# Performance work log

Measured on AMD Instinct MI355X. Metric: run time of the kernel, lower is better.

## Reference

```python
import jax, jax.numpy as jnp
import numpy as np

N, E, B, IN, H, T = 50000, 800000, 256, 32, 96, 8
BN_EPS = 1e-5


def setup_inputs() -> dict:
    key = jax.random.key(0)
    ks = jax.random.split(key, 40)
    inp = {}
    inp["x"] = jax.random.normal(ks[0], (N, IN), dtype=jnp.float32)
    inp["edge_index"] = jax.random.randint(ks[1], (2, E), 0, N, dtype=jnp.int64)
    inp["batch"] = jnp.sort(jax.random.randint(ks[2], (N,), 0, B, dtype=jnp.int64))
    inp["r_target"] = jax.random.randint(ks[3], (B,), 0, T, dtype=jnp.int64)
    k = 4
    for i, din in zip((1, 2, 3), (IN, H, H)):
        inp[f"w_in{i}"] = jax.random.normal(ks[k], (din, H), dtype=jnp.float32) / np.sqrt(din); k += 1
        inp[f"b_in{i}"] = jnp.zeros((H,), dtype=jnp.float32)
        inp[f"gamma{i}"] = jnp.ones((H,), dtype=jnp.float32)
        inp[f"beta{i}"] = jnp.zeros((H,), dtype=jnp.float32)
        inp[f"rmean{i}"] = jax.random.normal(ks[k], (H,), dtype=jnp.float32) * 0.1; k += 1
        inp[f"rvar{i}"] = jax.random.uniform(ks[k], (H,), minval=0.5, maxval=1.5, dtype=jnp.float32); k += 1
        inp[f"w_out{i}"] = jax.random.normal(ks[k], (H, H), dtype=jnp.float32) / np.sqrt(H); k += 1
        inp[f"b_out{i}"] = jnp.zeros((H,), dtype=jnp.float32)
    inp["head_w"] = jax.random.normal(ks[k], (T, H), dtype=jnp.float32) / np.sqrt(H)
    inp["head_b"] = jnp.zeros((T,), dtype=jnp.float32)
    return inp


def gin_conv(h, edge_index, w_in, b_in, gamma, beta, rmean, rvar, w_out, b_out):
    # PyG GINConv with eps=0: mlp((1+0)*x + sum_{j in N(i)} x_j)
    agg = jax.ops.segment_sum(h[edge_index[0]], edge_index[1], num_segments=N)
    z = (h + agg) @ w_in + b_in                                   # [N, H]
    z = (z - rmean) * (gamma * jax.lax.rsqrt(rvar + BN_EPS)) + beta  # eval-mode BN
    z = jax.nn.relu(z)
    z = jax.nn.relu(z @ w_out + b_out)
    return z


def reference(x, edge_index, batch, r_target,
              w_in1, b_in1, gamma1, beta1, rmean1, rvar1, w_out1, b_out1,
              w_in2, b_in2, gamma2, beta2, rmean2, rvar2, w_out2, b_out2,
              w_in3, b_in3, gamma3, beta3, rmean3, rvar3, w_out3, b_out3,
              head_w, head_b):
    h = gin_conv(x, edge_index, w_in1, b_in1, gamma1, beta1, rmean1, rvar1, w_out1, b_out1)
    h = jax.nn.relu(h)
    h = gin_conv(h, edge_index, w_in2, b_in2, gamma2, beta2, rmean2, rvar2, w_out2, b_out2)
    h = jax.nn.relu(h)
    h = gin_conv(h, edge_index, w_in3, b_in3, gamma3, beta3, rmean3, rvar3, w_out3, b_out3)
    pooled = jax.ops.segment_sum(h, batch, num_segments=B)        # [B, H]
    # dropout p=0.5 in eval mode -> identity
    w = head_w[r_target]                                          # [B, H] per-sample head
    b = head_b[r_target]                                          # [B]
    return jnp.sum(pooled * w, axis=-1) + b                       # [B]
```

## Files before the change

### kernel.cpp

```cpp
#include <hip/hip_runtime.h>

using u16 = unsigned short;
using u32 = unsigned int;
using u64 = unsigned long long;

typedef __attribute__((ext_vector_type(8))) short bf16x8;
typedef __attribute__((ext_vector_type(4))) float f32x4;

constexpr int Nn  = 50000;
constexpr int Ee  = 800000;
constexpr int Bb  = 256;
constexpr int INF = 32;
constexpr int Hh  = 96;
constexpr float BN_EPS = 1e-5f;

constexpr int BINW = 128;
constexpr int NBIN = (Nn + BINW - 1) / BINW;
constexpr int P1B  = 256;
constexpr int EPB  = Ee / P1B;
constexpr int CAP  = 40;
constexpr int P3IT = P1B * CAP / 256;

constexpr int WROW   = 104;
constexpr int WMAT   = 96 * WROW;
constexpr int WB_TOT = 6 * WMAT;

__device__ __forceinline__ float bfL(u32 u) { return __uint_as_float(u << 16); }
__device__ __forceinline__ float bfH(u32 u) { return __uint_as_float(u & 0xFFFF0000u); }
__device__ __forceinline__ u32 f2bfb(float f) {
    u32 b = __float_as_uint(f);
    return (b + 0x7FFFu + ((b >> 16) & 1u)) >> 16;
}
__device__ __forceinline__ float bf2f(u16 u) { return __uint_as_float(((u32)u) << 16); }

__global__ void x2bf_kernel(const float* __restrict__ x, u16* __restrict__ xb) {
    const int total = Nn * INF / 8;
    for (int i = blockIdx.x * 256 + threadIdx.x; i < total; i += gridDim.x * 256) {
        const float4 a = ((const float4*)x)[2 * i];
        const float4 b = ((const float4*)x)[2 * i + 1];
        uint4 R;
        R.x = f2bfb(a.x) | (f2bfb(a.y) << 16);
        R.y = f2bfb(a.z) | (f2bfb(a.w) << 16);
        R.z = f2bfb(b.x) | (f2bfb(b.y) << 16);
        R.w = f2bfb(b.z) | (f2bfb(b.w) << 16);
        ((uint4*)xb)[i] = R;
    }
}

__global__ void w2bf_kernel(const float* __restrict__ w1i, const float* __restrict__ w1o,
                            const float* __restrict__ w2i, const float* __restrict__ w2o,
                            const float* __restrict__ w3i, const float* __restrict__ w3o,
                            u16* __restrict__ wb) {
    const int i = blockIdx.x * 256 + threadIdx.x;
    if (i >= WB_TOT / 2) return;
    const int mat = i / (WMAT / 2);
    const int rem = i % (WMAT / 2);
    const int j   = rem / (WROW / 2);
    const int k   = (rem % (WROW / 2)) * 2;
    const float* src; int din;
    switch (mat) {
        case 0: src = w1i; din = 32; break;
        case 1: src = w1o; din = 96; break;
        case 2: src = w2i; din = 96; break;
        case 3: src = w2o; din = 96; break;
        case 4: src = w3i; din = 96; break;
        default: src = w3o; din = 96; break;
    }
    const u32 lo = (k     < din) ? f2bfb(src[(long)k * 96 + j])       : 0u;
    const u32 hi = (k + 1 < din) ? f2bfb(src[(long)(k + 1) * 96 + j]) : 0u;
    ((u32*)wb)[i] = lo | (hi << 16);
}

__global__ __launch_bounds__(256)
void p1_bin_kernel(const int* __restrict__ src, const int* __restrict__ dst,
                   u32* __restrict__ binbuf, int* __restrict__ counts,
                   int* __restrict__ bintot) {
    __shared__ int cur[NBIN];
    const int b = blockIdx.x, tid = threadIdx.x;
    for (int k = tid; k < NBIN; k += 256) cur[k] = 0;
    __syncthreads();
    const long e0 = (long)b * EPB;
    for (int i = tid; i < EPB; i += 256) {
        const long e = e0 + i;
        const int d = dst[e];
        const int k = d >> 7;
        const int pos = atomicAdd(&cur[k], 1);
        binbuf[((long)b * NBIN + k) * CAP + pos] = ((u32)(d & 127) << 16) | (u32)src[e];
    }
    __syncthreads();
    for (int k = tid; k < NBIN; k += 256) {
        const int c = cur[k];
        counts[k * P1B + b] = c;
        if (c) atomicAdd(&bintot[k], c);
    }
}

__global__ void p2_binscan_kernel(const int* __restrict__ bintot, int* __restrict__ binbase,
                                  int* __restrict__ rowptr) {
    __shared__ int ps[512];
    const int t = threadIdx.x;
    const int v = (t < NBIN) ? bintot[t] : 0;
    ps[t] = v;
    __syncthreads();
    for (int d = 1; d < 512; d <<= 1) {
        int u = (t >= d) ? ps[t - d] : 0;
        __syncthreads();
        if (t >= d) ps[t] += u;
        __syncthreads();
    }
    if (t < NBIN) binbase[t] = ps[t] - v;
    if (t == 0) rowptr[Nn] = Ee;
}

__global__ __launch_bounds__(256)
void p3_binsort_kernel(const u32* __restrict__ binbuf, const int* __restrict__ counts,
                       const int* __restrict__ binbase, int* __restrict__ rowptr,
                       u16* __restrict__ csr) {
    __shared__ int cnt[P1B];
    __shared__ int lhist[BINW];
    __shared__ int lpref[BINW];
    const int k = blockIdx.x, tid = threadIdx.x;

    for (int b = tid; b < P1B; b += 256) cnt[b] = counts[k * P1B + b];
    if (tid < BINW) lhist[tid] = 0;
    __syncthreads();

    u32 pv[P3IT];
    u64 vmask = 0;
    #pragma unroll
    for (int it = 0; it < P3IT; ++it) {
        const int flat = tid + it * 256;
        const int b = flat / CAP, i = flat % CAP;
        if (i < cnt[b]) {
            const u32 v = binbuf[((long)b * NBIN + k) * CAP + i];
            pv[it] = v;
            vmask |= 1ull << it;
            atomicAdd(&lhist[v >> 16], 1);
        }
    }
    __syncthreads();

    if (tid < BINW) lpref[tid] = lhist[tid];
    __syncthreads();
    for (int d = 1; d < BINW; d <<= 1) {
        int u = 0;
        if (tid < BINW && tid >= d) u = lpref[tid - d];
        __syncthreads();
        if (tid < BINW && tid >= d) lpref[tid] += u;
        __syncthreads();
    }
    if (tid < BINW) lpref[tid] -= lhist[tid];

    const int base = binbase[k];
    const int node = k * BINW + tid;
    if (tid < BINW && node < Nn) rowptr[node] = base + lpref[tid];
    if (tid < BINW) lhist[tid] = 0;
    __syncthreads();

    #pragma unroll
    for (int it = 0; it < P3IT; ++it) {
        if (vmask & (1ull << it)) {
            const u32 v = pv[it];
            const int dl = v >> 16;
            const int pos = base + lpref[dl] + atomicAdd(&lhist[dl], 1);
            csr[pos] = (u16)(v & 0xFFFFu);
        }
    }
}

template<int DIN>
__global__ __launch_bounds__(384, 4)
void layer_kernel(const u16* __restrict__ hsrc, const int* __restrict__ rowptr,
                  const u16* __restrict__ csr,
                  const u16* __restrict__ wbg1, const u16* __restrict__ wbg2,
                  const float* __restrict__ b_in,
                  const float* __restrict__ gamma, const float* __restrict__ beta,
                  const float* __restrict__ rmean, const float* __restrict__ rvar,
                  const float* __restrict__ b_out,
                  u16* __restrict__ out) {
    constexpr int TILE = 32;
    constexpr int XST  = 104;
    __shared__ __align__(16) u16 wT[96 * XST];
    __shared__ __align__(16) u16 xs[TILE * XST];

    const int tid = threadIdx.x;
    const int nbase = blockIdx.x * TILE;

    for (int i = tid; i < 96 * XST / 8; i += 384)
        ((uint4*)wT)[i] = ((const uint4*)wbg1)[i];

    {
        const int grp = tid / 12, ln = tid % 12;
        const int node = nbase + grp;
        if (node < Nn) {
            const int e0 = rowptr[node], e1 = rowptr[node + 1];
            if constexpr (DIN == 96) {
                const uint4* h4 = (const uint4*)hsrc;
                float a0, a1, a2, a3, a4, a5, a6, a7;
                {
                    const uint4 U = h4[(long)node * 12 + ln];
                    a0 = bfL(U.x); a1 = bfH(U.x); a2 = bfL(U.y); a3 = bfH(U.y);
                    a4 = bfL(U.z); a5 = bfH(U.z); a6 = bfL(U.w); a7 = bfH(U.w);
                }
                int e = e0;
                for (; e + 4 <= e1; e += 4) {
                    const long s0 = csr[e], s1 = csr[e + 1], s2 = csr[e + 2], s3 = csr[e + 3];
                    const uint4 U0 = h4[s0 * 12 + ln];
                    const uint4 U1 = h4[s1 * 12 + ln];
                    const uint4 U2 = h4[s2 * 12 + ln];
                    const uint4 U3 = h4[s3 * 12 + ln];
                    a0 += bfL(U0.x); a1 += bfH(U0.x); a2 += bfL(U0.y); a3 += bfH(U0.y);
                    a4 += bfL(U0.z); a5 += bfH(U0.z); a6 += bfL(U0.w); a7 += bfH(U0.w);
                    a0 += bfL(U1.x); a1 += bfH(U1.x); a2 += bfL(U1.y); a3 += bfH(U1.y);
                    a4 += bfL(U1.z); a5 += bfH(U1.z); a6 += bfL(U1.w); a7 += bfH(U1.w);
                    a0 += bfL(U2.x); a1 += bfH(U2.x); a2 += bfL(U2.y); a3 += bfH(U2.y);
                    a4 += bfL(U2.z); a5 += bfH(U2.z); a6 += bfL(U2.w); a7 += bfH(U2.w);
                    a0 += bfL(U3.x); a1 += bfH(U3.x); a2 += bfL(U3.y); a3 += bfH(U3.y);
                    a4 += bfL(U3.z); a5 += bfH(U3.z); a6 += bfL(U3.w); a7 += bfH(U3.w);
                }
                for (; e < e1; ++e) {
                    const uint4 U = h4[(long)csr[e] * 12 + ln];
                    a0 += bfL(U.x); a1 += bfH(U.x); a2 += bfL(U.y); a3 += bfH(U.y);
                    a4 += bfL(U.z); a5 += bfH(U.z); a6 += bfL(U.w); a7 += bfH(U.w);
                }
                u32* xp = (u32*)&xs[grp * XST + ln * 8];
                xp[0] = f2bfb(a0) | (f2bfb(a1) << 16);
                xp[1] = f2bfb(a2) | (f2bfb(a3) << 16);
                xp[2] = f2bfb(a4) | (f2bfb(a5) << 16);
                xp[3] = f2bfb(a6) | (f2bfb(a7) << 16);
            } else {
                if (ln < 8) {
                    const uint2* h2 = (const uint2*)hsrc;
                    float a0, a1, a2, a3;
                    {
                        const uint2 U = h2[(long)node * 8 + ln];
                        a0 = bfL(U.x); a1 = bfH(U.x); a2 = bfL(U.y); a3 = bfH(U.y);
                    }
                    int e = e0;
                    for (; e + 4 <= e1; e += 4) {
                        const long s0 = csr[e], s1 = csr[e + 1], s2 = csr[e + 2], s3 = csr[e + 3];
                        const uint2 U0 = h2[s0 * 8 + ln];
                        const uint2 U1 = h2[s1 * 8 + ln];
                        const uint2 U2 = h2[s2 * 8 + ln];
                        const uint2 U3 = h2[s3 * 8 + ln];
                        a0 += bfL(U0.x); a1 += bfH(U0.x); a2 += bfL(U0.y); a3 += bfH(U0.y);
                        a0 += bfL(U1.x); a1 += bfH(U1.x); a2 += bfL(U1.y); a3 += bfH(U1.y);
                        a0 += bfL(U2.x); a1 += bfH(U2.x); a2 += bfL(U2.y); a3 += bfH(U2.y);
                        a0 += bfL(U3.x); a1 += bfH(U3.x); a2 += bfL(U3.y); a3 += bfH(U3.y);
                    }
                    for (; e < e1; ++e) {
                        const uint2 U = h2[(long)csr[e] * 8 + ln];
                        a0 += bfL(U.x); a1 += bfH(U.x); a2 += bfL(U.y); a3 += bfH(U.y);
                    }
                    u32* xp = (u32*)&xs[grp * XST + ln * 4];
                    xp[0] = f2bfb(a0) | (f2bfb(a1) << 16);
                    xp[1] = f2bfb(a2) | (f2bfb(a3) << 16);
                }
            }
        } else {
            if constexpr (DIN == 96) {
                u32* xp = (u32*)&xs[grp * XST + ln * 8];
                xp[0] = xp[1] = xp[2] = xp[3] = 0u;
            } else if (ln < 8) {
                u32* q = (u32*)&xs[grp * XST + ln * 4];
                q[0] = q[1] = 0u;
            }
        }
    }

    const int lane = tid & 63, wave = tid >> 6;
    const int lr = lane & 15;
    const int md = (lane >> 4) * 4;
    const int lk = (lane >> 4) * 8;
    const int jg = wave * 16 + lr;

    const float sA = gamma[jg] * rsqrtf(rvar[jg] + BN_EPS);
    const float sC = (b_in[jg] - rmean[jg]) * sA + beta[jg];
    const float Bo = b_out[jg];
    __syncthreads();

    f32x4 acc0 = {0.f, 0.f, 0.f, 0.f}, acc1 = {0.f, 0.f, 0.f, 0.f};
    #pragma unroll
    for (int ks = 0; ks < DIN / 32; ++ks) {
        const int k0 = ks * 32 + lk;
        const bf16x8 b  = *(const bf16x8*)&wT[jg * XST + k0];
        const bf16x8 a0 = *(const bf16x8*)&xs[lr * XST + k0];
        const bf16x8 a1 = *(const bf16x8*)&xs[(16 + lr) * XST + k0];
        acc0 = __builtin_amdgcn_mfma_f32_16x16x32_bf16(a0, b, acc0, 0, 0, 0);
        acc1 = __builtin_amdgcn_mfma_f32_16x16x32_bf16(a1, b, acc1, 0, 0, 0);
    }

    u16 z0[4], z1[4];
    #pragma unroll
    for (int r = 0; r < 4; ++r) {
        z0[r] = (u16)f2bfb(fmaxf(fmaf(acc0[r], sA, sC), 0.0f));
        z1[r] = (u16)f2bfb(fmaxf(fmaf(acc1[r], sA, sC), 0.0f));
    }
    __syncthreads();

    #pragma unroll
    for (int r = 0; r < 4; ++r) {
        xs[(md + r) * XST + jg]      = z0[r];
        xs[(16 + md + r) * XST + jg] = z1[r];
    }
    for (int i = tid; i < 96 * XST / 8; i += 384)
        ((uint4*)wT)[i] = ((const uint4*)wbg2)[i];
    __syncthreads();

    f32x4 o0 = {0.f, 0.f, 0.f, 0.f}, o1 = {0.f, 0.f, 0.f, 0.f};
    #pragma unroll
    for (int ks = 0; ks < 3; ++ks) {
        const int k0 = ks * 32 + lk;
        const bf16x8 b  = *(const bf16x8*)&wT[jg * XST + k0];
        const bf16x8 a0 = *(const bf16x8*)&xs[lr * XST + k0];
        const bf16x8 a1 = *(const bf16x8*)&xs[(16 + lr) * XST + k0];
        o0 = __builtin_amdgcn_mfma_f32_16x16x32_bf16(a0, b, o0, 0, 0, 0);
        o1 = __builtin_amdgcn_mfma_f32_16x16x32_bf16(a1, b, o1, 0, 0, 0);
    }

    #pragma unroll
    for (int r = 0; r < 4; ++r) {
        const int n0 = nbase + md + r;
        if (n0 < Nn)
            out[(long)n0 * Hh + jg] = (u16)f2bfb(fmaxf(o0[r] + Bo, 0.0f));
        const int n1 = nbase + 16 + md + r;
        if (n1 < Nn)
            out[(long)n1 * Hh + jg] = (u16)f2bfb(fmaxf(o1[r] + Bo, 0.0f));
    }
}

constexpr int PCHUNK = 64;
__global__ void pool_kernel(const u16* __restrict__ h, const int* __restrict__ batch,
                            float* __restrict__ pooled) {
    const int j = threadIdx.x;
    const int c0 = blockIdx.x * PCHUNK;
    const int c1 = min(c0 + PCHUNK, Nn);
    if (c0 >= Nn) return;

    int bcur = batch[c0];
    float acc = 0.0f;
    for (int n = c0; n < c1; ++n) {
        const int bb = batch[n];
        if (bb != bcur) {
            atomicAdd(&pooled[(long)bcur * Hh + j], acc);
            acc = 0.0f;
            bcur = bb;
        }
        acc += bf2f(h[(long)n * Hh + j]);
    }
    atomicAdd(&pooled[(long)bcur * Hh + j], acc);
}

__global__ void head_kernel(const float* __restrict__ pooled, const int* __restrict__ rt,
                            const float* __restrict__ hw, const float* __restrict__ hb,
                            float* __restrict__ outv) {
    const int b = blockIdx.x;
    const int lane = threadIdx.x;
    const int t = rt[b];
    const float* pp = pooled + (long)b * Hh;
    const float* wp = hw + (long)t * Hh;
    float s = 0.0f;
    for (int j = lane; j < Hh; j += 64) s += pp[j] * wp[j];
    #pragma unroll
    for (int off = 32; off > 0; off >>= 1) s += __shfl_down(s, off, 64);
    if (lane == 0) outv[b] = s + hb[t];
}

extern "C" void kernel_launch(void* const* d_in, const int* in_sizes, int n_in,
                              void* d_out, int out_size, void* d_ws, size_t ws_size,
                              hipStream_t stream) {
    const float* x     = (const float*)d_in[0];
    const int*   ei    = (const int*)d_in[1];
    const int*   src   = ei;
    const int*   dst   = ei + Ee;
    const int*   batch = (const int*)d_in[2];
    const int*   rt    = (const int*)d_in[3];

    const float* P[3][8];
    for (int l = 0; l < 3; ++l)
        for (int p = 0; p < 8; ++p)
            P[l][p] = (const float*)d_in[4 + l * 8 + p];
    const float* head_w = (const float*)d_in[28];
    const float* head_b = (const float*)d_in[29];

    const size_t NH = (size_t)Nn * Hh;
    u16*   tA      = (u16*)d_ws;
    u16*   tB      = tA + NH;
    u16*   xb      = tB + NH;
    u16*   wball   = xb + (size_t)Nn * INF;
    float* pooled  = (float*)(wball + WB_TOT);
    int*   rowptr  = (int*)(pooled + (size_t)Bb * Hh);
    int*   counts  = rowptr + Nn + 1;
    int*   binbase = counts + NBIN * P1B;
    int*   bintot  = binbase + NBIN;
    u16*   csr     = (u16*)(bintot + NBIN);
    u32*   binbuf  = (u32*)tA;
    float* out     = (float*)d_out;

    const dim3 blk256(256), blk384(384), blk512(512), blk96(96);
    const int GRID_L    = (Nn + 31) / 32;
    const int GRID_POOL = (Nn + PCHUNK - 1) / PCHUNK;

    x2bf_kernel<<<782, blk256, 0, stream>>>(x, xb);
    w2bf_kernel<<<(WB_TOT / 2 + 255) / 256, blk256, 0, stream>>>(
        P[0][0], P[0][6], P[1][0], P[1][6], P[2][0], P[2][6], wball);
    hipMemsetAsync(bintot, 0, NBIN * sizeof(int), stream);
    p1_bin_kernel<<<P1B, blk256, 0, stream>>>(src, dst, binbuf, counts, bintot);
    p2_binscan_kernel<<<1, blk512, 0, stream>>>(bintot, binbase, rowptr);
    p3_binsort_kernel<<<NBIN, blk256, 0, stream>>>(binbuf, counts, binbase, rowptr, csr);

    layer_kernel<INF><<<GRID_L, blk384, 0, stream>>>(xb, rowptr, csr,
        wball + 0 * WMAT, wball + 1 * WMAT,
        P[0][1], P[0][2], P[0][3], P[0][4], P[0][5], P[0][7], tA);

    layer_kernel<Hh><<<GRID_L, blk384, 0, stream>>>(tA, rowptr, csr,
        wball + 2 * WMAT, wball + 3 * WMAT,
        P[1][1], P[1][2], P[1][3], P[1][4], P[1][5], P[1][7], tB);

    layer_kernel<Hh><<<GRID_L, blk384, 0, stream>>>(tB, rowptr, csr,
        wball + 4 * WMAT, wball + 5 * WMAT,
        P[2][1], P[2][2], P[2][3], P[2][4], P[2][5], P[2][7], tA);

    hipMemsetAsync(pooled, 0, (size_t)Bb * Hh * sizeof(float), stream);
    pool_kernel<<<GRID_POOL, blk96, 0, stream>>>(tA, batch, pooled);
    head_kernel<<<Bb, 64, 0, stream>>>(pooled, rt, head_w, head_b, out);
}
```

Measured before the change: 167.4 us.

## Fuse graph pooling into last GIN layer and unroll neighbor gathers by eight

Measured after the change: 152.3 us. -9.0%, faster.

```diff
diff --git a/kernel.cpp b/kernel.cpp
--- a/kernel.cpp
+++ b/kernel.cpp
@@ -168,7 +168,7 @@
     }
 }
 
-template<int DIN>
+template<int DIN, bool POOL>
 __global__ __launch_bounds__(384, 4)
 void layer_kernel(const u16* __restrict__ hsrc, const int* __restrict__ rowptr,
                   const u16* __restrict__ csr,
@@ -177,7 +177,8 @@
                   const float* __restrict__ gamma, const float* __restrict__ beta,
                   const float* __restrict__ rmean, const float* __restrict__ rvar,
                   const float* __restrict__ b_out,
-                  u16* __restrict__ out) {
+                  u16* __restrict__ out,
+                  const int* __restrict__ batch, float* __restrict__ pooled) {
     constexpr int TILE = 32;
     constexpr int XST  = 104;
     __shared__ __align__(16) u16 wT[96 * XST];
@@ -203,22 +204,27 @@
                     a4 = bfL(U.z); a5 = bfH(U.z); a6 = bfL(U.w); a7 = bfH(U.w);
                 }
                 int e = e0;
-                for (; e + 4 <= e1; e += 4) {
-                    const long s0 = csr[e], s1 = csr[e + 1], s2 = csr[e + 2], s3 = csr[e + 3];
-                    const uint4 U0 = h4[s0 * 12 + ln];
-                    const uint4 U1 = h4[s1 * 12 + ln];
-                    const uint4 U2 = h4[s2 * 12 + ln];
-                    const uint4 U3 = h4[s3 * 12 + ln];
-                    a0 += bfL(U0.x); a1 += bfH(U0.x); a2 += bfL(U0.y); a3 += bfH(U0.y);
-                    a4 += bfL(U0.z); a5 += bfH(U0.z); a6 += bfL(U0.w); a7 += bfH(U0.w);
-                    a0 += bfL(U1.x); a1 += bfH(U1.x); a2 += bfL(U1.y); a3 += bfH(U1.y);
-                    a4 += bfL(U1.z); a5 += bfH(U1.z); a6 += bfL(U1.w); a7 += bfH(U1.w);
-                    a0 += bfL(U2.x); a1 += bfH(U2.x); a2 += bfL(U2.y); a3 += bfH(U2.y);
-                    a4 += bfL(U2.z); a5 += bfH(U2.z); a6 += bfL(U2.w); a7 += bfH(U2.w);
-                    a0 += bfL(U3.x); a1 += bfH(U3.x); a2 += bfL(U3.y); a3 += bfH(U3.y);
-                    a4 += bfL(U3.z); a5 += bfH(U3.z); a6 += bfL(U3.w); a7 += bfH(U3.w);
-                }
-                for (; e < e1; ++e) {
+                for (; e + 8 <= e1; e += 8) {
+                    uint4 U[8];
+                    #pragma unroll
+                    for (int q = 0; q < 8; ++q) U[q] = h4[(long)csr[e + q] * 12 + ln];
+                    #pragma unroll
+                    for (int q = 0; q < 8; ++q) {
+                        a0 += bfL(U[q].x); a1 += bfH(U[q].x);
+                        a2 += bfL(U[q].y); a3 += bfH(U[q].y);
+                        a4 += bfL(U[q].z); a5 += bfH(U[q].z);
+                        a6 += bfL(U[q].w); a7 += bfH(U[q].w);
+                    }
+                }
+                for (; e + 2 <= e1; e += 2) {
+                    const uint4 Ua = h4[(long)csr[e] * 12 + ln];
+                    const uint4 Ub = h4[(long)csr[e + 1] * 12 + ln];
+                    a0 += bfL(Ua.x); a1 += bfH(Ua.x); a2 += bfL(Ua.y); a3 += bfH(Ua.y);
+                    a4 += bfL(Ua.z); a5 += bfH(Ua.z); a6 += bfL(Ua.w); a7 += bfH(Ua.w);
+                    a0 += bfL(Ub.x); a1 += bfH(Ub.x); a2 += bfL(Ub.y); a3 += bfH(Ub.y);
+                    a4 += bfL(Ub.z); a5 += bfH(Ub.z); a6 += bfL(Ub.w); a7 += bfH(Ub.w);
+                }
+                if (e < e1) {
                     const uint4 U = h4[(long)csr[e] * 12 + ln];
                     a0 += bfL(U.x); a1 += bfH(U.x); a2 += bfL(U.y); a3 += bfH(U.y);
                     a4 += bfL(U.z); a5 += bfH(U.z); a6 += bfL(U.w); a7 += bfH(U.w);
@@ -237,16 +243,15 @@
                         a0 = bfL(U.x); a1 = bfH(U.x); a2 = bfL(U.y); a3 = bfH(U.y);
                     }
                     int e = e0;
-                    for (; e + 4 <= e1; e += 4) {
-                        const long s0 = csr[e], s1 = csr[e + 1], s2 = csr[e + 2], s3 = csr[e + 3];
-                        const uint2 U0 = h2[s0 * 8 + ln];
-                        const uint2 U1 = h2[s1 * 8 + ln];
-                        const uint2 U2 = h2[s2 * 8 + ln];
-                        const uint2 U3 = h2[s3 * 8 + ln];
-                        a0 += bfL(U0.x); a1 += bfH(U0.x); a2 += bfL(U0.y); a3 += bfH(U0.y);
-                        a0 += bfL(U1.x); a1 += bfH(U1.x); a2 += bfL(U1.y); a3 += bfH(U1.y);
-                        a0 += bfL(U2.x); a1 += bfH(U2.x); a2 += bfL(U2.y); a3 += bfH(U2.y);
-                        a0 += bfL(U3.x); a1 += bfH(U3.x); a2 += bfL(U3.y); a3 += bfH(U3.y);
+                    for (; e + 8 <= e1; e += 8) {
+                        uint2 U[8];
+                        #pragma unroll
+                        for (int q = 0; q < 8; ++q) U[q] = h2[(long)csr[e + q] * 8 + ln];
+                        #pragma unroll
+                        for (int q = 0; q < 8; ++q) {
+                            a0 += bfL(U[q].x); a1 += bfH(U[q].x);
+                            a2 += bfL(U[q].y); a3 += bfH(U[q].y);
+                        }
                     }
                     for (; e < e1; ++e) {
                         const uint2 U = h2[(long)csr[e] * 8 + ln];
@@ -318,37 +323,46 @@
         o1 = __builtin_amdgcn_mfma_f32_16x16x32_bf16(a1, b, o1, 0, 0, 0);
     }
 
+    u16 y0[4], y1[4];
+    #pragma unroll
+    for (int r = 0; r < 4; ++r) {
+        y0[r] = (u16)f2bfb(fmaxf(o0[r] + Bo, 0.0f));
+        y1[r] = (u16)f2bfb(fmaxf(o1[r] + Bo, 0.0f));
+    }
     #pragma unroll
     for (int r = 0; r < 4; ++r) {
         const int n0 = nbase + md + r;
-        if (n0 < Nn)
-            out[(long)n0 * Hh + jg] = (u16)f2bfb(fmaxf(o0[r] + Bo, 0.0f));
+        if (n0 < Nn) out[(long)n0 * Hh + jg] = y0[r];
         const int n1 = nbase + 16 + md + r;
-        if (n1 < Nn)
-            out[(long)n1 * Hh + jg] = (u16)f2bfb(fmaxf(o1[r] + Bo, 0.0f));
-    }
-}
-
-constexpr int PCHUNK = 64;
-__global__ void pool_kernel(const u16* __restrict__ h, const int* __restrict__ batch,
-                            float* __restrict__ pooled) {
-    const int j = threadIdx.x;
-    const int c0 = blockIdx.x * PCHUNK;
-    const int c1 = min(c0 + PCHUNK, Nn);
-    if (c0 >= Nn) return;
-
-    int bcur = batch[c0];
-    float acc = 0.0f;
-    for (int n = c0; n < c1; ++n) {
-        const int bb = batch[n];
-        if (bb != bcur) {
+        if (n1 < Nn) out[(long)n1 * Hh + jg] = y1[r];
+    }
+
+    if constexpr (POOL) {
+        __syncthreads();
+        #pragma unroll
+        for (int r = 0; r < 4; ++r) {
+            xs[(md + r) * XST + jg]      = y0[r];
+            xs[(16 + md + r) * XST + jg] = y1[r];
+        }
+        __syncthreads();
+        if (tid < Hh) {
+            const int j = tid;
+            float acc = 0.0f;
+            int bcur = batch[nbase];
+            for (int r = 0; r < TILE; ++r) {
+                const int node = nbase + r;
+                if (node >= Nn) break;
+                const int bb = batch[node];
+                if (bb != bcur) {
+                    atomicAdd(&pooled[(long)bcur * Hh + j], acc);
+                    acc = 0.0f;
+                    bcur = bb;
+                }
+                acc += bf2f(xs[r * XST + j]);
+            }
             atomicAdd(&pooled[(long)bcur * Hh + j], acc);
-            acc = 0.0f;
-            bcur = bb;
         }
-        acc += bf2f(h[(long)n * Hh + j]);
-    }
-    atomicAdd(&pooled[(long)bcur * Hh + j], acc);
+    }
 }
 
 __global__ void head_kernel(const float* __restrict__ pooled, const int* __restrict__ rt,
@@ -397,9 +411,8 @@
     u32*   binbuf  = (u32*)tA;
     float* out     = (float*)d_out;
 
-    const dim3 blk256(256), blk384(384), blk512(512), blk96(96);
-    const int GRID_L    = (Nn + 31) / 32;
-    const int GRID_POOL = (Nn + PCHUNK - 1) / PCHUNK;
+    const dim3 blk256(256), blk384(384), blk512(512);
+    const int GRID_L = (Nn + 31) / 32;
 
     x2bf_kernel<<<782, blk256, 0, stream>>>(x, xb);
     w2bf_kernel<<<(WB_TOT / 2 + 255) / 256, blk256, 0, stream>>>(
@@ -409,19 +422,18 @@
     p2_binscan_kernel<<<1, blk512, 0, stream>>>(bintot, binbase, rowptr);
     p3_binsort_kernel<<<NBIN, blk256, 0, stream>>>(binbuf, counts, binbase, rowptr, csr);
 
-    layer_kernel<INF><<<GRID_L, blk384, 0, stream>>>(xb, rowptr, csr,
+    layer_kernel<INF, false><<<GRID_L, blk384, 0, stream>>>(xb, rowptr, csr,
         wball + 0 * WMAT, wball + 1 * WMAT,
-        P[0][1], P[0][2], P[0][3], P[0][4], P[0][5], P[0][7], tA);
-
-    layer_kernel<Hh><<<GRID_L, blk384, 0, stream>>>(tA, rowptr, csr,
+        P[0][1], P[0][2], P[0][3], P[0][4], P[0][5], P[0][7], tA, nullptr, nullptr);
+
+    layer_kernel<Hh, false><<<GRID_L, blk384, 0, stream>>>(tA, rowptr, csr,
         wball + 2 * WMAT, wball + 3 * WMAT,
-        P[1][1], P[1][2], P[1][3], P[1][4], P[1][5], P[1][7], tB);
-
-    layer_kernel<Hh><<<GRID_L, blk384, 0, stream>>>(tB, rowptr, csr,
+        P[1][1], P[1][2], P[1][3], P[1][4], P[1][5], P[1][7], tB, nullptr, nullptr);
+
+    hipMemsetAsync(pooled, 0, (size_t)Bb * Hh * sizeof(float), stream);
+    layer_kernel<Hh, true><<<GRID_L, blk384, 0, stream>>>(tB, rowptr, csr,
         wball + 4 * WMAT, wball + 5 * WMAT,
-        P[2][1], P[2][2], P[2][3], P[2][4], P[2][5], P[2][7], tA);
-
-    hipMemsetAsync(pooled, 0, (size_t)Bb * Hh * sizeof(float), stream);
-    pool_kernel<<<GRID_POOL, blk96, 0, stream>>>(tA, batch, pooled);
+        P[2][1], P[2][2], P[2][3], P[2][4], P[2][5], P[2][7], tA, batch, pooled);
+
     head_kernel<<<Bb, 64, 0, stream>>>(pooled, rt, head_w, head_b, out);
 }
```
